# Kernel tuning notes

Hardware: AMD Instinct MI355X
Metric: run time of the kernel (lower is better)

Reference implementation:

```python
import jax, jax.numpy as jnp
import numpy as np
from jax import lax

T, B, V, E, HID, K = 512, 256, 50000, 300, 512, 9
H = HID // 2  # per-direction LSTM hidden size


def setup_inputs() -> dict:
    key = jax.random.key(0)
    ks = jax.random.split(key, 16)
    input_ids = jax.random.randint(ks[0], (T, B), 0, V, dtype=jnp.int32)
    lens = jax.random.randint(ks[1], (B,), T // 2, T + 1, dtype=jnp.int32)
    seq_lengths = jnp.sort(lens)[::-1].at[0].set(T)  # sorted desc, max == T
    label_ids = jax.random.randint(ks[2], (T, B), 0, K, dtype=jnp.int32)
    s = 0.1
    emb_table = jax.random.normal(ks[3], (V, E), jnp.float32) * s
    W_ih_f = jax.random.normal(ks[4], (4 * H, E), jnp.float32) * s
    W_hh_f = jax.random.normal(ks[5], (4 * H, H), jnp.float32) * s
    b_f = jax.random.normal(ks[6], (4 * H,), jnp.float32) * s  # b_ih + b_hh fused
    W_ih_b = jax.random.normal(ks[7], (4 * H, E), jnp.float32) * s
    W_hh_b = jax.random.normal(ks[8], (4 * H, H), jnp.float32) * s
    b_b = jax.random.normal(ks[9], (4 * H,), jnp.float32) * s
    W_out = jax.random.normal(ks[10], (K, HID), jnp.float32) * s
    b_out = jax.random.normal(ks[11], (K,), jnp.float32) * s
    start_trans = jax.random.normal(ks[12], (K,), jnp.float32) * s
    end_trans = jax.random.normal(ks[13], (K,), jnp.float32) * s
    trans = jax.random.normal(ks[14], (K, K), jnp.float32) * s
    return dict(input_ids=input_ids, seq_lengths=seq_lengths, label_ids=label_ids,
                emb_table=emb_table, W_ih_f=W_ih_f, W_hh_f=W_hh_f, b_f=b_f,
                W_ih_b=W_ih_b, W_hh_b=W_hh_b, b_b=b_b, W_out=W_out, b_out=b_out,
                start_trans=start_trans, end_trans=end_trans, trans=trans)


def _run_lstm(x, maskf, W_ih, W_hh, b, reverse):
    # x: [T,B,E], maskf: [T,B] float. Precompute input projections (one big GEMM).
    xg = jnp.einsum('tbe,ge->tbg', x, W_ih) + b  # [T,B,4H]

    def step(carry, inp):
        h, c = carry
        xg_t, m = inp
        gates = xg_t + h @ W_hh.T
        i, f, g, o = jnp.split(gates, 4, axis=-1)
        c_new = jax.nn.sigmoid(f) * c + jax.nn.sigmoid(i) * jnp.tanh(g)
        h_new = jax.nn.sigmoid(o) * jnp.tanh(c_new)
        m = m[:, None]
        return (m * h_new + (1 - m) * h, m * c_new + (1 - m) * c), m * h_new + (1 - m) * h

    init = (jnp.zeros((B, H), x.dtype), jnp.zeros((B, H), x.dtype))
    _, hs = lax.scan(step, init, (xg, maskf), reverse=reverse)
    return hs  # [T,B,H]


def reference(input_ids, seq_lengths, label_ids, emb_table, W_ih_f, W_hh_f, b_f,
              W_ih_b, W_hh_b, b_b, W_out, b_out, start_trans, end_trans, trans):
    maskf = (jnp.arange(T)[:, None] < seq_lengths[None, :]).astype(emb_table.dtype)  # [T,B]
    maskb = maskf.astype(bool)

    embeds = emb_table[input_ids]  # [T,B,E]
    h_f = _run_lstm(embeds, maskf, W_ih_f, W_hh_f, b_f, reverse=False)
    h_b = _run_lstm(embeds, maskf, W_ih_b, W_hh_b, b_b, reverse=True)
    lstm_out = jnp.concatenate([h_f, h_b], axis=-1)  # [T,B,HID]
    emissions = jnp.einsum('tbh,kh->tbk', lstm_out, W_out) + b_out  # [T,B,K]

    b_idx = jnp.arange(B)
    # --- CRF numerator (gold path score) ---
    num = start_trans[label_ids[0]] + emissions[0, b_idx, label_ids[0]]
    trans_sc = trans[label_ids[:-1], label_ids[1:]]  # [T-1,B]
    emit_sc = jnp.take_along_axis(emissions[1:], label_ids[1:, :, None], axis=2)[..., 0]
    num = num + jnp.sum((trans_sc + emit_sc) * maskf[1:], axis=0)
    last_tags = label_ids[seq_lengths - 1, b_idx]
    num = num + end_trans[last_tags]

    # --- CRF denominator (forward algorithm, log-sum-exp scan) ---
    def fwd_step(alpha, inp):
        em_t, m = inp
        nxt = jax.nn.logsumexp(alpha[:, :, None] + trans[None], axis=1) + em_t
        return jnp.where(m[:, None].astype(bool), nxt, alpha), None

    alpha0 = start_trans[None] + emissions[0]  # [B,K]
    alpha, _ = lax.scan(fwd_step, alpha0, (emissions[1:], maskf[1:]))
    denom = jax.nn.logsumexp(alpha + end_trans[None], axis=1)
    loss = -jnp.sum(num - denom)  # torchcrf reduction='sum', model negates llh

    # --- Viterbi decode ---
    def vit_step(score, inp):
        em_t, m = inp
        brd = score[:, :, None] + trans[None]  # [B,K_prev,K_next]
        idx = jnp.argmax(brd, axis=1)          # [B,K]
        nxt = jnp.max(brd, axis=1) + em_t
        return jnp.where(m[:, None].astype(bool), nxt, score), idx

    score0 = start_trans[None] + emissions[0]
    score, hist = lax.scan(vit_step, score0, (emissions[1:], maskf[1:]))  # hist [T-1,B,K]
    best_last = jnp.argmax(score + end_trans[None], axis=1)  # [B] tag at last valid pos

    def back_step(tag, inp):
        h_t, m_next = inp
        new = jnp.where(m_next.astype(bool),
                        jnp.take_along_axis(h_t, tag[:, None], axis=1)[:, 0],
                        best_last)
        return new, new

    _, preds = lax.scan(back_step, best_last, (hist, maskf[1:]), reverse=True)  # [T-1,B]
    pred_ids = jnp.concatenate([preds, best_last[None]], axis=0)  # [T,B]
    pred_ids = jnp.where(maskb, pred_ids, 0)
    return loss, pred_ids
```

## Files before the change

kernel.cpp:

```cpp
#include <hip/hip_runtime.h>
#include <math.h>

#define TT 512
#define BB 256
#define EE 300
#define KK 9
#define HH 256
#define GG 1024
#define CHS 64
#define NCH (TT/CHS)

#define OFF_XG ((size_t)0)
#define OFF_WT (OFF_XG + (size_t)2*CHS*BB*GG)
#define OFF_HS (OFF_WT + (size_t)2*64*1024*4)
#define OFF_CS (OFF_HS + (size_t)2*BB*HH)
#define OFF_EF (OFF_CS + (size_t)2*BB*HH)
#define OFF_EB (OFF_EF + (size_t)BB*TT*KK)
#define OFF_ND (OFF_EB + (size_t)BB*TT*KK)

#define DOT4(a_,b_) ((a_).x*(b_).x + (a_).y*(b_).y + (a_).z*(b_).z + (a_).w*(b_).w)
#define FMA4(acc_, w_, h_) do { \
    acc_ = fmaf((w_).x, (h_).x, acc_); \
    acc_ = fmaf((w_).y, (h_).y, acc_); \
    acc_ = fmaf((w_).z, (h_).z, acc_); \
    acc_ = fmaf((w_).w, (h_).w, acc_); } while (0)

__global__ __launch_bounds__(1024) void wtrans_kernel(
    const float* __restrict__ Wf, const float* __restrict__ Wb, float* __restrict__ Wt)
{
  int idx = blockIdx.x * 1024 + threadIdx.x;
  int dir = idx >> 16;
  int r   = (idx >> 6) & 1023;
  int k4  = idx & 63;
  const float* W = dir ? Wb : Wf;
  float4 v = *(const float4*)&W[(size_t)r * HH + k4 * 4];
  ((float4*)Wt)[(size_t)dir * 65536 + (size_t)k4 * 1024 + r] = v;
}

__global__ __launch_bounds__(256) void gemm_xg_kernel(
    const int* __restrict__ ids, const float* __restrict__ emb,
    const float* __restrict__ W_ih_f, const float* __restrict__ W_ih_b,
    const float* __restrict__ b_f, const float* __restrict__ b_b,
    float* __restrict__ xgc, int ci)
{
  __shared__ float As[60][132];
  __shared__ float Ws[60][132];
  __shared__ int tokid[128];
  const int tid = threadIdx.x;
  const int dir = blockIdx.x >> 7;
  const int r   = blockIdx.x & 127;
  const float* W_ih = dir ? W_ih_b : W_ih_f;
  const float* bias = dir ? b_b : b_f;

  if (tid < 128) {
    int m = r * 128 + tid;
    int sidx = ci * CHS + (m >> 8);
    int t = dir ? (TT - 1 - sidx) : sidx;
    tokid[tid] = ids[t * BB + (m & 255)];
  }
  __syncthreads();

  const int ty = tid >> 4, tx = tid & 15;
  for (int nt = 0; nt < 8; ++nt) {
    float acc[8][8];
    #pragma unroll
    for (int a_ = 0; a_ < 8; ++a_)
      #pragma unroll
      for (int b_ = 0; b_ < 8; ++b_) acc[a_][b_] = 0.f;

    for (int kc = 0; kc < 5; ++kc) {
      __syncthreads();
      for (int i = tid; i < 128 * 15; i += 256) {
        int mm = i / 15, kq = i - mm * 15;
        float4 v = *(const float4*)&emb[(size_t)tokid[mm] * EE + kc * 60 + kq * 4];
        As[kq*4+0][mm] = v.x; As[kq*4+1][mm] = v.y;
        As[kq*4+2][mm] = v.z; As[kq*4+3][mm] = v.w;
      }
      for (int i = tid; i < 128 * 15; i += 256) {
        int nn = i / 15, kq = i - nn * 15;
        float4 v = *(const float4*)&W_ih[(size_t)(nt*128+nn) * EE + kc * 60 + kq * 4];
        Ws[kq*4+0][nn] = v.x; Ws[kq*4+1][nn] = v.y;
        Ws[kq*4+2][nn] = v.z; Ws[kq*4+3][nn] = v.w;
      }
      __syncthreads();
      for (int kk = 0; kk < 60; ++kk) {
        float4 a0 = *(const float4*)&As[kk][ty*8];
        float4 a1 = *(const float4*)&As[kk][ty*8+4];
        float4 w0 = *(const float4*)&Ws[kk][tx*8];
        float4 w1 = *(const float4*)&Ws[kk][tx*8+4];
        float av[8] = {a0.x,a0.y,a0.z,a0.w,a1.x,a1.y,a1.z,a1.w};
        float wv8[8] = {w0.x,w0.y,w0.z,w0.w,w1.x,w1.y,w1.z,w1.w};
        #pragma unroll
        for (int im = 0; im < 8; ++im)
          #pragma unroll
          for (int in = 0; in < 8; ++in) acc[im][in] += av[im] * wv8[in];
      }
    }
    #pragma unroll
    for (int im = 0; im < 8; ++im) {
      int m = ty*8 + im;
      int n = nt*128 + tx*8;
      float4 o0, o1;
      o0.x = acc[im][0] + bias[n+0]; o0.y = acc[im][1] + bias[n+1];
      o0.z = acc[im][2] + bias[n+2]; o0.w = acc[im][3] + bias[n+3];
      o1.x = acc[im][4] + bias[n+4]; o1.y = acc[im][5] + bias[n+5];
      o1.z = acc[im][6] + bias[n+6]; o1.w = acc[im][7] + bias[n+7];
      float* dst = &xgc[(size_t)(dir*16384 + r*128 + m) * GG + n];
      *(float4*)dst = o0; *(float4*)(dst+4) = o1;
    }
  }
}

__global__ __launch_bounds__(1024, 1) void rec_chunk_kernel(
    const float* __restrict__ xgc, const float* __restrict__ Wt,
    const int* __restrict__ lens,
    float* __restrict__ hst, float* __restrict__ cst,
    float* __restrict__ emisf, float* __restrict__ emisb,
    const float* __restrict__ W_out, const float* __restrict__ b_out, int ci)
{
  __shared__ __align__(16) float hring[2][2][272];
  __shared__ __align__(16) float Wo[KK][256];

  const int tid  = threadIdx.x;
  const int bid  = blockIdx.x;
  const int dir  = (bid & 7) >> 2;
  const int grp  = (bid >> 3) * 4 + (bid & 3);
  const int b0   = grp * 2;
  const int lane = tid & 63;
  const int wv   = tid >> 6;
  const int rg   = wv * 16 + (lane & 15);
  const int kseg = (lane >> 4) & 3;
  const bool cellLane = (lane & 48) == 0;
  float* emis = dir ? emisb : emisf;

  for (int i = tid; i < KK * 64; i += 1024) {
    int k = i >> 6, q = i & 63;
    *(float4*)&Wo[k][q*4] = *(const float4*)&W_out[(size_t)k * 512 + dir*256 + q*4];
  }

  int eb = 0, ek = 0, es = 0;
  const bool edo = tid < 2 * KK * 16;
  if (edo) { int q = tid; eb = q / 144; q -= eb * 144; ek = q >> 4; es = q & 15; }
  const float ebias = (edo && dir == 0) ? b_out[ek] : 0.f;

  int len2[2];
  #pragma unroll
  for (int b = 0; b < 2; ++b) len2[b] = lens[b0 + b];

  float creg[2] = {0.f,0.f}, hreg[2] = {0.f,0.f};
  if (cellLane) {
    if (ci > 0) {
      #pragma unroll
      for (int b = 0; b < 2; ++b) {
        hreg[b] = hst[((size_t)dir*BB + b0 + b) * HH + rg];
        creg[b] = cst[((size_t)dir*BB + b0 + b) * HH + rg];
      }
    }
    #pragma unroll
    for (int b = 0; b < 2; ++b)
      hring[0][b][rg + ((rg >> 6) << 2)] = hreg[b];
  }
  __syncthreads();

  const float4* wp = (const float4*)Wt + (size_t)dir * 65536
                   + (size_t)(kseg * 16) * 1024 + rg;

  for (int sl = 0; sl < CHS; ++sl) {
    const int s = ci * CHS + sl;
    const int t = dir ? (TT - 1 - s) : s;
    const int cur = sl & 1, nxt = cur ^ 1;

    float xv[4][2];
    if (cellLane) {
      const float* xb = xgc + ((size_t)dir*(CHS*BB) + (size_t)sl*BB + b0) * GG + rg;
      #pragma unroll
      for (int q = 0; q < 4; ++q)
        #pragma unroll
        for (int b = 0; b < 2; ++b)
          xv[q][b] = __builtin_nontemporal_load(&xb[(size_t)b * GG + q * 256]);
    }

    float acc[4][2];
    #pragma unroll
    for (int q = 0; q < 4; ++q) { acc[q][0] = 0.f; acc[q][1] = 0.f; }

    const float4* hb = (const float4*)&hring[0][0][0] + cur * (2*68) + kseg * 17;
    float4 w0 = wp[0], w1 = wp[256], w2 = wp[512], w3 = wp[768];
    #pragma unroll 5
    for (int i = 0; i < 15; ++i) {
      const float4* wn = wp + (size_t)(i + 1) * 1024;
      float4 n0 = wn[0], n1 = wn[256], n2 = wn[512], n3 = wn[768];
      float4 h0 = hb[i], h1 = hb[68 + i];
      FMA4(acc[0][0], w0, h0); FMA4(acc[0][1], w0, h1);
      FMA4(acc[1][0], w1, h0); FMA4(acc[1][1], w1, h1);
      FMA4(acc[2][0], w2, h0); FMA4(acc[2][1], w2, h1);
      FMA4(acc[3][0], w3, h0); FMA4(acc[3][1], w3, h1);
      w0 = n0; w1 = n1; w2 = n2; w3 = n3;
    }
    {
      float4 h0 = hb[15], h1 = hb[68 + 15];
      FMA4(acc[0][0], w0, h0); FMA4(acc[0][1], w0, h1);
      FMA4(acc[1][0], w1, h0); FMA4(acc[1][1], w1, h1);
      FMA4(acc[2][0], w2, h0); FMA4(acc[2][1], w2, h1);
      FMA4(acc[3][0], w3, h0); FMA4(acc[3][1], w3, h1);
    }

    #pragma unroll
    for (int q = 0; q < 4; ++q)
      #pragma unroll
      for (int b = 0; b < 2; ++b) {
        float v = acc[q][b];
        v += __shfl_xor(v, 16);
        v += __shfl_xor(v, 32);
        acc[q][b] = v;
      }

    if (cellLane) {
      #pragma unroll
      for (int b = 0; b < 2; ++b) {
        float gi = acc[0][b] + xv[0][b];
        float gf = acc[1][b] + xv[1][b];
        float gg = acc[2][b] + xv[2][b];
        float go = acc[3][b] + xv[3][b];
        float si = 1.f / (1.f + expf(-gi));
        float sf = 1.f / (1.f + expf(-gf));
        float so = 1.f / (1.f + expf(-go));
        float cn = sf * creg[b] + si * tanhf(gg);
        float hn = so * tanhf(cn);
        bool m = t < len2[b];
        hreg[b] = m ? hn : hreg[b];
        creg[b] = m ? cn : creg[b];
        hring[nxt][b][rg + ((rg >> 6) << 2)] = hreg[b];
      }
    }
    __syncthreads();

    if (edo) {
      float r = 0.f;
      #pragma unroll
      for (int i4 = 0; i4 < 4; ++i4) {
        float4 h4 = *(const float4*)&hring[nxt][eb][es*4 + i4*68];
        float4 w4 = *(const float4*)&Wo[ek][es*4 + i4*64];
        r += DOT4(h4, w4);
      }
      r += __shfl_xor(r, 8); r += __shfl_xor(r, 4);
      r += __shfl_xor(r, 2); r += __shfl_xor(r, 1);
      if (es == 0)
        __builtin_nontemporal_store(r + ebias,
            &emis[((size_t)(b0 + eb) * TT + t) * KK + ek]);
    }
  }

  if (cellLane) {
    #pragma unroll
    for (int b = 0; b < 2; ++b) {
      hst[((size_t)dir*BB + b0 + b) * HH + rg] = hreg[b];
      cst[((size_t)dir*BB + b0 + b) * HH + rg] = creg[b];
    }
  }
}

__global__ __launch_bounds__(64) void crf_kernel(
    const float* __restrict__ emis_f, const float* __restrict__ emis_b2,
    const int* __restrict__ labels, const int* __restrict__ lens,
    const float* __restrict__ start_trans, const float* __restrict__ end_trans,
    const float* __restrict__ trans,
    float* __restrict__ numden, float* __restrict__ outp)
{
  const int b = blockIdx.x;
  const int lane = threadIdx.x;
  __shared__ __align__(16) float em[TT * KK];
  __shared__ unsigned char hist[TT * KK];
  const float4* ef = (const float4*)(emis_f + (size_t)b * TT * KK);
  const float4* eb = (const float4*)(emis_b2 + (size_t)b * TT * KK);
  for (int i = lane; i < TT*KK/4; i += 64) {
    float4 a = ef[i], c = eb[i];
    float4 o; o.x = a.x+c.x; o.y = a.y+c.y; o.z = a.z+c.z; o.w = a.w+c.w;
    ((float4*)em)[i] = o;
  }
  const int len = lens[b];
  const int k = lane < KK ? lane : KK-1;
  float tc[KK];
  #pragma unroll
  for (int jj = 0; jj < KK; ++jj) tc[jj] = trans[jj*KK + k];
  __syncthreads();

  float nacc = 0.f;
  for (int t = lane; t < TT; t += 64) {
    int lt = labels[t*BB + b];
    if (t == 0) nacc += start_trans[lt] + em[lt];
    else if (t < len) nacc += trans[labels[(t-1)*BB + b]*KK + lt] + em[t*KK + lt];
  }
  if (lane == 0) nacc += end_trans[labels[(size_t)(len-1)*BB + b]];
  #pragma unroll
  for (int off = 32; off; off >>= 1) nacc += __shfl_down(nacc, off);

  float alpha[KK], score[KK];
  #pragma unroll
  for (int jj = 0; jj < KK; ++jj) {
    float v = start_trans[jj] + em[jj];
    alpha[jj] = v; score[jj] = v;
  }
  for (int t = 1; t < TT; ++t) {
    float av[KK]; float mx = -1e30f;
    #pragma unroll
    for (int jj = 0; jj < KK; ++jj) { av[jj] = alpha[jj] + tc[jj]; mx = fmaxf(mx, av[jj]); }
    float ssum = 0.f;
    #pragma unroll
    for (int jj = 0; jj < KK; ++jj) ssum += expf(av[jj] - mx);
    float e_tk = em[t*KK + k];
    float na = mx + logf(ssum) + e_tk;
    float best = -1e30f; int bj = 0;
    #pragma unroll
    for (int jj = 0; jj < KK; ++jj) {
      float sv = score[jj] + tc[jj];
      if (sv > best) { best = sv; bj = jj; }
    }
    float ns = best + e_tk;
    bool msk = t < len;
    na = msk ? na : alpha[k];
    ns = msk ? ns : score[k];
    if (lane < KK) hist[(t-1)*KK + lane] = (unsigned char)bj;
    #pragma unroll
    for (int jj = 0; jj < KK; ++jj) { alpha[jj] = __shfl(na, jj); score[jj] = __shfl(ns, jj); }
  }
  float dm = -1e30f;
  #pragma unroll
  for (int jj = 0; jj < KK; ++jj) dm = fmaxf(dm, alpha[jj] + end_trans[jj]);
  float dsum = 0.f;
  #pragma unroll
  for (int jj = 0; jj < KK; ++jj) dsum += expf(alpha[jj] + end_trans[jj] - dm);
  float denom = dm + logf(dsum);
  int bl_ = 0; float bs = -1e30f;
  #pragma unroll
  for (int jj = 0; jj < KK; ++jj) {
    float v = score[jj] + end_trans[jj];
    if (v > bs) { bs = v; bl_ = jj; }
  }
  if (lane == 0) numden[b] = nacc - denom;
  __syncthreads();
  if (lane == 0) {
    int tag = bl_;
    outp[1 + (size_t)(TT-1)*BB + b] = ((TT-1) < len) ? (float)bl_ : 0.f;
    for (int s = TT-2; s >= 0; --s) {
      tag = ((s+1) < len) ? (int)hist[s*KK + tag] : bl_;
      outp[1 + (size_t)s*BB + b] = (s < len) ? (float)tag : 0.f;
    }
  }
}

__global__ __launch_bounds__(256) void loss_reduce_kernel(
    const float* __restrict__ numden, float* __restrict__ out)
{
  __shared__ float sh[256];
  int tid = threadIdx.x;
  sh[tid] = numden[tid];
  __syncthreads();
  for (int s = 128; s > 0; s >>= 1) {
    if (tid < s) sh[tid] += sh[tid + s];
    __syncthreads();
  }
  if (tid == 0) out[0] = -sh[0];
}

extern "C" void kernel_launch(void* const* d_in, const int* in_sizes, int n_in,
                              void* d_out, int out_size, void* d_ws, size_t ws_size,
                              hipStream_t stream)
{
  const int*   ids    = (const int*)d_in[0];
  const int*   lens   = (const int*)d_in[1];
  const int*   labels = (const int*)d_in[2];
  const float* emb    = (const float*)d_in[3];
  const float* W_ih_f = (const float*)d_in[4];
  const float* W_hh_f = (const float*)d_in[5];
  const float* b_f    = (const float*)d_in[6];
  const float* W_ih_b = (const float*)d_in[7];
  const float* W_hh_b = (const float*)d_in[8];
  const float* b_b    = (const float*)d_in[9];
  const float* W_out  = (const float*)d_in[10];
  const float* b_out  = (const float*)d_in[11];
  const float* s_tr   = (const float*)d_in[12];
  const float* e_tr   = (const float*)d_in[13];
  const float* trans  = (const float*)d_in[14];
  float* out = (float*)d_out;

  float* ws = (float*)d_ws;
  float* xgc    = ws + OFF_XG;
  float* Wt     = ws + OFF_WT;
  float* hst    = ws + OFF_HS;
  float* cst    = ws + OFF_CS;
  float* emis_f = ws + OFF_EF;
  float* emis_b = ws + OFF_EB;
  float* numden = ws + OFF_ND;

  wtrans_kernel<<<128, 1024, 0, stream>>>(W_hh_f, W_hh_b, Wt);

  for (int ci = 0; ci < NCH; ++ci) {
    gemm_xg_kernel<<<256, 256, 0, stream>>>(ids, emb, W_ih_f, W_ih_b, b_f, b_b, xgc, ci);
    rec_chunk_kernel<<<256, 1024, 0, stream>>>(xgc, Wt, lens, hst, cst,
                                               emis_f, emis_b, W_out, b_out, ci);
  }

  crf_kernel<<<BB, 64, 0, stream>>>(emis_f, emis_b, labels, lens, s_tr, e_tr, trans, numden, out);
  loss_reduce_kernel<<<1, 256, 0, stream>>>(numden, out);
}
```

Measured before the change: 8.374 ms.

## Precompute vocab-level input projections and run LSTM recurrence in one persistent kernel

Instead of projecting gathered embeddings per time chunk, the code precomputes emb_table·W_ihᵀ+b for all 50000 vocabulary rows and both directions into a large workspace table. A single persistent recurrence kernel then gathers the gate inputs by token id at each step, which removes the eight chunked launches and their hidden/cell state save and restore. This path needs about 400MB of workspace and runs only when the workspace is large enough. The vocab GEMM (V=50000) does more FLOPs than projecting the T·B=131072 tokens directly.

```diff
diff --git a/kernel.cpp b/kernel.cpp
--- a/kernel.cpp
+++ b/kernel.cpp
@@ -7,6 +7,7 @@
 #define KK 9
 #define HH 256
 #define GG 1024
+#define VV 50000
 #define CHS 64
 #define NCH (TT/CHS)
 
@@ -18,6 +19,13 @@
 #define OFF_EB (OFF_EF + (size_t)BB*TT*KK)
 #define OFF_ND (OFF_EB + (size_t)BB*TT*KK)
 
+#define OFF_EW  ((size_t)0)
+#define OFF_WT2 (OFF_EW + (size_t)2*VV*GG)
+#define OFF_EF2 (OFF_WT2 + (size_t)2*64*1024*4)
+#define OFF_EB2 (OFF_EF2 + (size_t)BB*TT*KK)
+#define OFF_ND2 (OFF_EB2 + (size_t)BB*TT*KK)
+#define EW_WS_FLOATS (OFF_ND2 + 256)
+
 #define DOT4(a_,b_) ((a_).x*(b_).x + (a_).y*(b_).y + (a_).z*(b_).z + (a_).w*(b_).w)
 #define FMA4(acc_, w_, h_) do { \
     acc_ = fmaf((w_).x, (h_).x, acc_); \
@@ -35,6 +43,214 @@
   const float* W = dir ? Wb : Wf;
   float4 v = *(const float4*)&W[(size_t)r * HH + k4 * 4];
   ((float4*)Wt)[(size_t)dir * 65536 + (size_t)k4 * 1024 + r] = v;
+}
+
+__global__ __launch_bounds__(256) void ew_gemm_kernel(
+    const float* __restrict__ emb,
+    const float* __restrict__ W_ih_f, const float* __restrict__ W_ih_b,
+    const float* __restrict__ b_f, const float* __restrict__ b_b,
+    float* __restrict__ EW)
+{
+  __shared__ float As[60][132];
+  __shared__ float Ws[60][132];
+  __shared__ int tokid[128];
+  const int tid = threadIdx.x;
+  const int dir = blockIdx.y;
+  const int r   = blockIdx.x;
+  const float* W_ih = dir ? W_ih_b : W_ih_f;
+  const float* bias = dir ? b_b : b_f;
+
+  if (tid < 128) {
+    int v = r * 128 + tid;
+    tokid[tid] = v < VV ? v : VV - 1;
+  }
+  __syncthreads();
+
+  const int ty = tid >> 4, tx = tid & 15;
+  for (int nt = 0; nt < 8; ++nt) {
+    float acc[8][8];
+    #pragma unroll
+    for (int a_ = 0; a_ < 8; ++a_)
+      #pragma unroll
+      for (int b_ = 0; b_ < 8; ++b_) acc[a_][b_] = 0.f;
+
+    for (int kc = 0; kc < 5; ++kc) {
+      __syncthreads();
+      for (int i = tid; i < 128 * 15; i += 256) {
+        int mm = i / 15, kq = i - mm * 15;
+        float4 v = *(const float4*)&emb[(size_t)tokid[mm] * EE + kc * 60 + kq * 4];
+        As[kq*4+0][mm] = v.x; As[kq*4+1][mm] = v.y;
+        As[kq*4+2][mm] = v.z; As[kq*4+3][mm] = v.w;
+      }
+      for (int i = tid; i < 128 * 15; i += 256) {
+        int nn = i / 15, kq = i - nn * 15;
+        float4 v = *(const float4*)&W_ih[(size_t)(nt*128+nn) * EE + kc * 60 + kq * 4];
+        Ws[kq*4+0][nn] = v.x; Ws[kq*4+1][nn] = v.y;
+        Ws[kq*4+2][nn] = v.z; Ws[kq*4+3][nn] = v.w;
+      }
+      __syncthreads();
+      for (int kk = 0; kk < 60; ++kk) {
+        float4 a0 = *(const float4*)&As[kk][ty*8];
+        float4 a1 = *(const float4*)&As[kk][ty*8+4];
+        float4 w0 = *(const float4*)&Ws[kk][tx*8];
+        float4 w1 = *(const float4*)&Ws[kk][tx*8+4];
+        float av[8] = {a0.x,a0.y,a0.z,a0.w,a1.x,a1.y,a1.z,a1.w};
+        float wv8[8] = {w0.x,w0.y,w0.z,w0.w,w1.x,w1.y,w1.z,w1.w};
+        #pragma unroll
+        for (int im = 0; im < 8; ++im)
+          #pragma unroll
+          for (int in = 0; in < 8; ++in) acc[im][in] += av[im] * wv8[in];
+      }
+    }
+    #pragma unroll
+    for (int im = 0; im < 8; ++im) {
+      int v = r*128 + ty*8 + im;
+      if (v < VV) {
+        int n = nt*128 + tx*8;
+        float4 o0, o1;
+        o0.x = acc[im][0] + bias[n+0]; o0.y = acc[im][1] + bias[n+1];
+        o0.z = acc[im][2] + bias[n+2]; o0.w = acc[im][3] + bias[n+3];
+        o1.x = acc[im][4] + bias[n+4]; o1.y = acc[im][5] + bias[n+5];
+        o1.z = acc[im][6] + bias[n+6]; o1.w = acc[im][7] + bias[n+7];
+        float* dst = &EW[((size_t)dir * VV + v) * GG + n];
+        *(float4*)dst = o0; *(float4*)(dst+4) = o1;
+      }
+    }
+  }
+}
+
+__global__ __launch_bounds__(1024, 1) void rec_full_kernel(
+    const float* __restrict__ EW, const float* __restrict__ Wt,
+    const int* __restrict__ ids, const int* __restrict__ lens,
+    float* __restrict__ emisf, float* __restrict__ emisb,
+    const float* __restrict__ W_out, const float* __restrict__ b_out)
+{
+  __shared__ __align__(16) float hring[2][2][272];
+  __shared__ __align__(16) float Wo[KK][256];
+
+  const int tid  = threadIdx.x;
+  const int bid  = blockIdx.x;
+  const int dir  = (bid & 7) >> 2;
+  const int grp  = (bid >> 3) * 4 + (bid & 3);
+  const int b0   = grp * 2;
+  const int lane = tid & 63;
+  const int wv   = tid >> 6;
+  const int rg   = wv * 16 + (lane & 15);
+  const int kseg = (lane >> 4) & 3;
+  const bool cellLane = (lane & 48) == 0;
+  float* emis = dir ? emisb : emisf;
+
+  for (int i = tid; i < KK * 64; i += 1024) {
+    int k = i >> 6, q = i & 63;
+    *(float4*)&Wo[k][q*4] = *(const float4*)&W_out[(size_t)k * 512 + dir*256 + q*4];
+  }
+
+  int eb = 0, ek = 0, es = 0;
+  const bool edo = tid < 2 * KK * 16;
+  if (edo) { int q = tid; eb = q / 144; q -= eb * 144; ek = q >> 4; es = q & 15; }
+  const float ebias = (edo && dir == 0) ? b_out[ek] : 0.f;
+
+  int len2[2];
+  #pragma unroll
+  for (int b = 0; b < 2; ++b) len2[b] = lens[b0 + b];
+
+  float creg[2] = {0.f,0.f}, hreg[2] = {0.f,0.f};
+  if (cellLane) {
+    #pragma unroll
+    for (int b = 0; b < 2; ++b)
+      hring[0][b][rg + ((rg >> 6) << 2)] = 0.f;
+  }
+  __syncthreads();
+
+  const float4* wp = (const float4*)Wt + (size_t)dir * 65536
+                   + (size_t)(kseg * 16) * 1024 + rg;
+
+  for (int s = 0; s < TT; ++s) {
+    const int t = dir ? (TT - 1 - s) : s;
+    const int cur = s & 1, nxt = cur ^ 1;
+
+    float xv[4][2];
+    if (cellLane) {
+      #pragma unroll
+      for (int b = 0; b < 2; ++b) {
+        int tok = ids[(size_t)t * BB + b0 + b];
+        const float* xb = EW + ((size_t)dir * VV + tok) * GG + rg;
+        #pragma unroll
+        for (int q = 0; q < 4; ++q)
+          xv[q][b] = __builtin_nontemporal_load(&xb[q * 256]);
+      }
+    }
+
+    float acc[4][2];
+    #pragma unroll
+    for (int q = 0; q < 4; ++q) { acc[q][0] = 0.f; acc[q][1] = 0.f; }
+
+    const float4* hb = (const float4*)&hring[0][0][0] + cur * (2*68) + kseg * 17;
+    float4 w0 = wp[0], w1 = wp[256], w2 = wp[512], w3 = wp[768];
+    #pragma unroll 5
+    for (int i = 0; i < 15; ++i) {
+      const float4* wn = wp + (size_t)(i + 1) * 1024;
+      float4 n0 = wn[0], n1 = wn[256], n2 = wn[512], n3 = wn[768];
+      float4 h0 = hb[i], h1 = hb[68 + i];
+      FMA4(acc[0][0], w0, h0); FMA4(acc[0][1], w0, h1);
+      FMA4(acc[1][0], w1, h0); FMA4(acc[1][1], w1, h1);
+      FMA4(acc[2][0], w2, h0); FMA4(acc[2][1], w2, h1);
+      FMA4(acc[3][0], w3, h0); FMA4(acc[3][1], w3, h1);
+      w0 = n0; w1 = n1; w2 = n2; w3 = n3;
+    }
+    {
+      float4 h0 = hb[15], h1 = hb[68 + 15];
+      FMA4(acc[0][0], w0, h0); FMA4(acc[0][1], w0, h1);
+      FMA4(acc[1][0], w1, h0); FMA4(acc[1][1], w1, h1);
+      FMA4(acc[2][0], w2, h0); FMA4(acc[2][1], w2, h1);
+      FMA4(acc[3][0], w3, h0); FMA4(acc[3][1], w3, h1);
+    }
+
+    #pragma unroll
+    for (int q = 0; q < 4; ++q)
+      #pragma unroll
+      for (int b = 0; b < 2; ++b) {
+        float v = acc[q][b];
+        v += __shfl_xor(v, 16);
+        v += __shfl_xor(v, 32);
+        acc[q][b] = v;
+      }
+
+    if (cellLane) {
+      #pragma unroll
+      for (int b = 0; b < 2; ++b) {
+        float gi = acc[0][b] + xv[0][b];
+        float gf = acc[1][b] + xv[1][b];
+        float gg = acc[2][b] + xv[2][b];
+        float go = acc[3][b] + xv[3][b];
+        float si = 1.f / (1.f + expf(-gi));
+        float sf = 1.f / (1.f + expf(-gf));
+        float so = 1.f / (1.f + expf(-go));
+        float cn = sf * creg[b] + si * tanhf(gg);
+        float hn = so * tanhf(cn);
+        bool m = t < len2[b];
+        hreg[b] = m ? hn : hreg[b];
+        creg[b] = m ? cn : creg[b];
+        hring[nxt][b][rg + ((rg >> 6) << 2)] = hreg[b];
+      }
+    }
+    __syncthreads();
+
+    if (edo) {
+      float r = 0.f;
+      #pragma unroll
+      for (int i4 = 0; i4 < 4; ++i4) {
+        float4 h4 = *(const float4*)&hring[nxt][eb][es*4 + i4*68];
+        float4 w4 = *(const float4*)&Wo[ek][es*4 + i4*64];
+        r += DOT4(h4, w4);
+      }
+      r += __shfl_xor(r, 8); r += __shfl_xor(r, 4);
+      r += __shfl_xor(r, 2); r += __shfl_xor(r, 1);
+      if (es == 0)
+        __builtin_nontemporal_store(r + ebias,
+            &emis[((size_t)(b0 + eb) * TT + t) * KK + ek]);
+    }
+  }
 }
 
 __global__ __launch_bounds__(256) void gemm_xg_kernel(
@@ -383,24 +599,39 @@
   const float* e_tr   = (const float*)d_in[13];
   const float* trans  = (const float*)d_in[14];
   float* out = (float*)d_out;
-
   float* ws = (float*)d_ws;
-  float* xgc    = ws + OFF_XG;
-  float* Wt     = ws + OFF_WT;
-  float* hst    = ws + OFF_HS;
-  float* cst    = ws + OFF_CS;
-  float* emis_f = ws + OFF_EF;
-  float* emis_b = ws + OFF_EB;
-  float* numden = ws + OFF_ND;
-
-  wtrans_kernel<<<128, 1024, 0, stream>>>(W_hh_f, W_hh_b, Wt);
-
-  for (int ci = 0; ci < NCH; ++ci) {
-    gemm_xg_kernel<<<256, 256, 0, stream>>>(ids, emb, W_ih_f, W_ih_b, b_f, b_b, xgc, ci);
-    rec_chunk_kernel<<<256, 1024, 0, stream>>>(xgc, Wt, lens, hst, cst,
-                                               emis_f, emis_b, W_out, b_out, ci);
-  }
-
-  crf_kernel<<<BB, 64, 0, stream>>>(emis_f, emis_b, labels, lens, s_tr, e_tr, trans, numden, out);
-  loss_reduce_kernel<<<1, 256, 0, stream>>>(numden, out);
-}
+
+  if (ws_size >= (size_t)EW_WS_FLOATS * sizeof(float)) {
+    float* EW     = ws + OFF_EW;
+    float* Wt     = ws + OFF_WT2;
+    float* emis_f = ws + OFF_EF2;
+    float* emis_b = ws + OFF_EB2;
+    float* numden = ws + OFF_ND2;
+
+    wtrans_kernel<<<128, 1024, 0, stream>>>(W_hh_f, W_hh_b, Wt);
+    ew_gemm_kernel<<<dim3(391, 2), 256, 0, stream>>>(emb, W_ih_f, W_ih_b, b_f, b_b, EW);
+    rec_full_kernel<<<256, 1024, 0, stream>>>(EW, Wt, ids, lens,
+                                              emis_f, emis_b, W_out, b_out);
+    crf_kernel<<<BB, 64, 0, stream>>>(emis_f, emis_b, labels, lens, s_tr, e_tr, trans,
+                                      numden, out);
+    loss_reduce_kernel<<<1, 256, 0, stream>>>(numden, out);
+  } else {
+    float* xgc    = ws + OFF_XG;
+    float* Wt     = ws + OFF_WT;
+    float* hst    = ws + OFF_HS;
+    float* cst    = ws + OFF_CS;
+    float* emis_f = ws + OFF_EF;
+    float* emis_b = ws + OFF_EB;
+    float* numden = ws + OFF_ND;
+
+    wtrans_kernel<<<128, 1024, 0, stream>>>(W_hh_f, W_hh_b, Wt);
+    for (int ci = 0; ci < NCH; ++ci) {
+      gemm_xg_kernel<<<256, 256, 0, stream>>>(ids, emb, W_ih_f, W_ih_b, b_f, b_b, xgc, ci);
+      rec_chunk_kernel<<<256, 1024, 0, stream>>>(xgc, Wt, lens, hst, cst,
+                                                 emis_f, emis_b, W_out, b_out, ci);
+    }
+    crf_kernel<<<BB, 64, 0, stream>>>(emis_f, emis_b, labels, lens, s_tr, e_tr, trans,
+                                      numden, out);
+    loss_reduce_kernel<<<1, 256, 0, stream>>>(numden, out);
+  }
+}
```

Measured after the change: 8.376 ms. No clear change (+0.0%).

## Pre-transpose W_ih, split xg GEMM over N tiles, deepen W_hh prefetch

Applied to the files above, without the earlier changes.

W_ih is transposed once into a k-major workspace layout. The input-projection GEMM then launches 2048 blocks, one per 128-column N tile, instead of 256 blocks looping over 8 N tiles, and reads weights straight from global memory rather than staging them in shared memory. This raises parallelism and cuts shared-memory traffic, but each block now re-gathers the embedding rows for its tile. The recurrent matvec also changes from a one-step to a two-step-ahead register prefetch of W_hh, which adds register pressure.

```diff
diff --git a/kernel.cpp b/kernel.cpp
--- a/kernel.cpp
+++ b/kernel.cpp
@@ -10,13 +10,14 @@
 #define CHS 64
 #define NCH (TT/CHS)
 
-#define OFF_XG ((size_t)0)
-#define OFF_WT (OFF_XG + (size_t)2*CHS*BB*GG)
-#define OFF_HS (OFF_WT + (size_t)2*64*1024*4)
-#define OFF_CS (OFF_HS + (size_t)2*BB*HH)
-#define OFF_EF (OFF_CS + (size_t)2*BB*HH)
-#define OFF_EB (OFF_EF + (size_t)BB*TT*KK)
-#define OFF_ND (OFF_EB + (size_t)BB*TT*KK)
+#define OFF_XG  ((size_t)0)
+#define OFF_WT  (OFF_XG + (size_t)2*CHS*BB*GG)
+#define OFF_WTI (OFF_WT + (size_t)2*64*1024*4)
+#define OFF_HS  (OFF_WTI + (size_t)2*EE*GG)
+#define OFF_CS  (OFF_HS + (size_t)2*BB*HH)
+#define OFF_EF  (OFF_CS + (size_t)2*BB*HH)
+#define OFF_EB  (OFF_EF + (size_t)BB*TT*KK)
+#define OFF_ND  (OFF_EB + (size_t)BB*TT*KK)
 
 #define DOT4(a_,b_) ((a_).x*(b_).x + (a_).y*(b_).y + (a_).z*(b_).z + (a_).w*(b_).w)
 #define FMA4(acc_, w_, h_) do { \
@@ -37,77 +38,92 @@
   ((float4*)Wt)[(size_t)dir * 65536 + (size_t)k4 * 1024 + r] = v;
 }
 
+__global__ __launch_bounds__(256) void wtrans_ih_kernel(
+    const float* __restrict__ Wf, const float* __restrict__ Wb, float* __restrict__ WtI)
+{
+  __shared__ float T[64][301];
+  const int tid = threadIdx.x;
+  const int dir = blockIdx.x >> 4;
+  const int rt  = blockIdx.x & 15;
+  const float* W = dir ? Wb : Wf;
+  for (int i = tid; i < 64 * 75; i += 256) {
+    int r = i / 75, c4 = i - r * 75;
+    float4 v = *(const float4*)&W[(size_t)(rt*64 + r) * EE + c4*4];
+    T[r][c4*4+0] = v.x; T[r][c4*4+1] = v.y; T[r][c4*4+2] = v.z; T[r][c4*4+3] = v.w;
+  }
+  __syncthreads();
+  for (int i = tid; i < EE * 16; i += 256) {
+    int rq = i & 15, k = i >> 4;
+    float4 o;
+    o.x = T[rq*4+0][k]; o.y = T[rq*4+1][k]; o.z = T[rq*4+2][k]; o.w = T[rq*4+3][k];
+    *(float4*)&WtI[((size_t)dir * EE + k) * GG + rt*64 + rq*4] = o;
+  }
+}
+
 __global__ __launch_bounds__(256) void gemm_xg_kernel(
     const int* __restrict__ ids, const float* __restrict__ emb,
-    const float* __restrict__ W_ih_f, const float* __restrict__ W_ih_b,
+    const float* __restrict__ WtI,
     const float* __restrict__ b_f, const float* __restrict__ b_b,
     float* __restrict__ xgc, int ci)
 {
   __shared__ float As[60][132];
-  __shared__ float Ws[60][132];
   __shared__ int tokid[128];
   const int tid = threadIdx.x;
-  const int dir = blockIdx.x >> 7;
-  const int r   = blockIdx.x & 127;
-  const float* W_ih = dir ? W_ih_b : W_ih_f;
+  const int bx  = blockIdx.x;
+  const int ntg = bx >> 8;
+  const int dir = (bx >> 7) & 1;
+  const int rt  = bx & 127;
   const float* bias = dir ? b_b : b_f;
+  const float* Wk = WtI + (size_t)dir * EE * GG;
 
   if (tid < 128) {
-    int m = r * 128 + tid;
+    int m = rt * 128 + tid;
     int sidx = ci * CHS + (m >> 8);
     int t = dir ? (TT - 1 - sidx) : sidx;
     tokid[tid] = ids[t * BB + (m & 255)];
   }
-  __syncthreads();
 
   const int ty = tid >> 4, tx = tid & 15;
-  for (int nt = 0; nt < 8; ++nt) {
-    float acc[8][8];
-    #pragma unroll
-    for (int a_ = 0; a_ < 8; ++a_)
-      #pragma unroll
-      for (int b_ = 0; b_ < 8; ++b_) acc[a_][b_] = 0.f;
-
-    for (int kc = 0; kc < 5; ++kc) {
-      __syncthreads();
-      for (int i = tid; i < 128 * 15; i += 256) {
-        int mm = i / 15, kq = i - mm * 15;
-        float4 v = *(const float4*)&emb[(size_t)tokid[mm] * EE + kc * 60 + kq * 4];
-        As[kq*4+0][mm] = v.x; As[kq*4+1][mm] = v.y;
-        As[kq*4+2][mm] = v.z; As[kq*4+3][mm] = v.w;
-      }
-      for (int i = tid; i < 128 * 15; i += 256) {
-        int nn = i / 15, kq = i - nn * 15;
-        float4 v = *(const float4*)&W_ih[(size_t)(nt*128+nn) * EE + kc * 60 + kq * 4];
-        Ws[kq*4+0][nn] = v.x; Ws[kq*4+1][nn] = v.y;
-        Ws[kq*4+2][nn] = v.z; Ws[kq*4+3][nn] = v.w;
-      }
-      __syncthreads();
-      for (int kk = 0; kk < 60; ++kk) {
-        float4 a0 = *(const float4*)&As[kk][ty*8];
-        float4 a1 = *(const float4*)&As[kk][ty*8+4];
-        float4 w0 = *(const float4*)&Ws[kk][tx*8];
-        float4 w1 = *(const float4*)&Ws[kk][tx*8+4];
-        float av[8] = {a0.x,a0.y,a0.z,a0.w,a1.x,a1.y,a1.z,a1.w};
-        float wv8[8] = {w0.x,w0.y,w0.z,w0.w,w1.x,w1.y,w1.z,w1.w};
+  float acc[8][8];
+  #pragma unroll
+  for (int a_ = 0; a_ < 8; ++a_)
+    #pragma unroll
+    for (int b_ = 0; b_ < 8; ++b_) acc[a_][b_] = 0.f;
+
+  for (int kc = 0; kc < 5; ++kc) {
+    __syncthreads();
+    for (int i = tid; i < 128 * 15; i += 256) {
+      int mm = i / 15, kq = i - mm * 15;
+      float4 v = *(const float4*)&emb[(size_t)tokid[mm] * EE + kc * 60 + kq * 4];
+      As[kq*4+0][mm] = v.x; As[kq*4+1][mm] = v.y;
+      As[kq*4+2][mm] = v.z; As[kq*4+3][mm] = v.w;
+    }
+    __syncthreads();
+    for (int kk = 0; kk < 60; ++kk) {
+      float4 a0 = *(const float4*)&As[kk][ty*8];
+      float4 a1 = *(const float4*)&As[kk][ty*8+4];
+      const float* wrow = Wk + (size_t)(kc*60 + kk) * GG + ntg*128 + tx*8;
+      float4 w0 = *(const float4*)wrow;
+      float4 w1 = *(const float4*)(wrow + 4);
+      float av[8]  = {a0.x,a0.y,a0.z,a0.w,a1.x,a1.y,a1.z,a1.w};
+      float wv8[8] = {w0.x,w0.y,w0.z,w0.w,w1.x,w1.y,w1.z,w1.w};
+      #pragma unroll
+      for (int im = 0; im < 8; ++im)
         #pragma unroll
-        for (int im = 0; im < 8; ++im)
-          #pragma unroll
-          for (int in = 0; in < 8; ++in) acc[im][in] += av[im] * wv8[in];
-      }
-    }
-    #pragma unroll
-    for (int im = 0; im < 8; ++im) {
-      int m = ty*8 + im;
-      int n = nt*128 + tx*8;
-      float4 o0, o1;
-      o0.x = acc[im][0] + bias[n+0]; o0.y = acc[im][1] + bias[n+1];
-      o0.z = acc[im][2] + bias[n+2]; o0.w = acc[im][3] + bias[n+3];
-      o1.x = acc[im][4] + bias[n+4]; o1.y = acc[im][5] + bias[n+5];
-      o1.z = acc[im][6] + bias[n+6]; o1.w = acc[im][7] + bias[n+7];
-      float* dst = &xgc[(size_t)(dir*16384 + r*128 + m) * GG + n];
-      *(float4*)dst = o0; *(float4*)(dst+4) = o1;
-    }
+        for (int in = 0; in < 8; ++in) acc[im][in] += av[im] * wv8[in];
+    }
+  }
+  #pragma unroll
+  for (int im = 0; im < 8; ++im) {
+    int m = ty*8 + im;
+    int n = ntg*128 + tx*8;
+    float4 o0, o1;
+    o0.x = acc[im][0] + bias[n+0]; o0.y = acc[im][1] + bias[n+1];
+    o0.z = acc[im][2] + bias[n+2]; o0.w = acc[im][3] + bias[n+3];
+    o1.x = acc[im][4] + bias[n+4]; o1.y = acc[im][5] + bias[n+5];
+    o1.z = acc[im][6] + bias[n+6]; o1.w = acc[im][7] + bias[n+7];
+    float* dst = &xgc[(size_t)(dir*16384 + rt*128 + m) * GG + n];
+    *(float4*)dst = o0; *(float4*)(dst+4) = o1;
   }
 }
 
@@ -185,24 +201,24 @@
     for (int q = 0; q < 4; ++q) { acc[q][0] = 0.f; acc[q][1] = 0.f; }
 
     const float4* hb = (const float4*)&hring[0][0][0] + cur * (2*68) + kseg * 17;
-    float4 w0 = wp[0], w1 = wp[256], w2 = wp[512], w3 = wp[768];
-    #pragma unroll 5
-    for (int i = 0; i < 15; ++i) {
-      const float4* wn = wp + (size_t)(i + 1) * 1024;
-      float4 n0 = wn[0], n1 = wn[256], n2 = wn[512], n3 = wn[768];
+    float4 wr[3][4];
+    #pragma unroll
+    for (int d = 0; d < 2; ++d) {
+      const float4* wn = wp + (size_t)d * 1024;
+      wr[d][0] = wn[0]; wr[d][1] = wn[256]; wr[d][2] = wn[512]; wr[d][3] = wn[768];
+    }
+    #pragma unroll
+    for (int i = 0; i < 16; ++i) {
+      if (i < 14) {
+        const float4* wn = wp + (size_t)(i + 2) * 1024;
+        wr[(i+2)%3][0] = wn[0];   wr[(i+2)%3][1] = wn[256];
+        wr[(i+2)%3][2] = wn[512]; wr[(i+2)%3][3] = wn[768];
+      }
       float4 h0 = hb[i], h1 = hb[68 + i];
-      FMA4(acc[0][0], w0, h0); FMA4(acc[0][1], w0, h1);
-      FMA4(acc[1][0], w1, h0); FMA4(acc[1][1], w1, h1);
-      FMA4(acc[2][0], w2, h0); FMA4(acc[2][1], w2, h1);
-      FMA4(acc[3][0], w3, h0); FMA4(acc[3][1], w3, h1);
-      w0 = n0; w1 = n1; w2 = n2; w3 = n3;
-    }
-    {
-      float4 h0 = hb[15], h1 = hb[68 + 15];
-      FMA4(acc[0][0], w0, h0); FMA4(acc[0][1], w0, h1);
-      FMA4(acc[1][0], w1, h0); FMA4(acc[1][1], w1, h1);
-      FMA4(acc[2][0], w2, h0); FMA4(acc[2][1], w2, h1);
-      FMA4(acc[3][0], w3, h0); FMA4(acc[3][1], w3, h1);
+      FMA4(acc[0][0], wr[i%3][0], h0); FMA4(acc[0][1], wr[i%3][0], h1);
+      FMA4(acc[1][0], wr[i%3][1], h0); FMA4(acc[1][1], wr[i%3][1], h1);
+      FMA4(acc[2][0], wr[i%3][2], h0); FMA4(acc[2][1], wr[i%3][2], h1);
+      FMA4(acc[3][0], wr[i%3][3], h0); FMA4(acc[3][1], wr[i%3][3], h1);
     }
 
     #pragma unroll
@@ -387,6 +403,7 @@
   float* ws = (float*)d_ws;
   float* xgc    = ws + OFF_XG;
   float* Wt     = ws + OFF_WT;
+  float* WtI    = ws + OFF_WTI;
   float* hst    = ws + OFF_HS;
   float* cst    = ws + OFF_CS;
   float* emis_f = ws + OFF_EF;
@@ -394,9 +411,10 @@
   float* numden = ws + OFF_ND;
 
   wtrans_kernel<<<128, 1024, 0, stream>>>(W_hh_f, W_hh_b, Wt);
+  wtrans_ih_kernel<<<32, 256, 0, stream>>>(W_ih_f, W_ih_b, WtI);
 
   for (int ci = 0; ci < NCH; ++ci) {
-    gemm_xg_kernel<<<256, 256, 0, stream>>>(ids, emb, W_ih_f, W_ih_b, b_f, b_b, xgc, ci);
+    gemm_xg_kernel<<<2048, 256, 0, stream>>>(ids, emb, WtI, b_f, b_b, xgc, ci);
     rec_chunk_kernel<<<256, 1024, 0, stream>>>(xgc, Wt, lens, hst, cst,
                                                emis_f, emis_b, W_out, b_out, ci);
   }
```

New measurement: 20.31 ms. 143% more time.
